# Optimization experiments

Measured on AMD Instinct MI355X. Metric: run time of the kernel, lower is better.

## Reference

```python
import jax, jax.numpy as jnp
import numpy as np

B, S, E, HID, NTR, NCAL, CW, VOCAB, POS = 4096, 201, 32, 512, 4, 8, 16, 32, 256
LN_EPS = 1e-5


def _ln(x, g, b):
    m = x.mean(-1, keepdims=True)
    v = ((x - m) ** 2).mean(-1, keepdims=True)
    return (x - m) * jax.lax.rsqrt(v + LN_EPS) * g + b


def setup_inputs() -> dict:
    key = jax.random.key(0)
    ks = jax.random.split(key, 24)
    g = lambda i, shape, s=0.1: (jax.random.normal(ks[i], shape, jnp.float32) * s)
    return dict(
        encoded_seq=jax.random.randint(ks[0], (B, S), 0, VOCAB, jnp.int32),
        experiment_id=jax.random.randint(ks[1], (B,), 0, NCAL, jnp.int32),
        tok_emb=g(2, (VOCAB, E), 1.0),
        pos_emb=g(3, (POS, E), 1.0),
        ln1_g=jnp.ones((NTR, E)), ln1_b=jnp.zeros((NTR, E)),
        wq=g(4, (NTR, E, E)), wk=g(5, (NTR, E, E)), wv=g(6, (NTR, E, E)),
        bq=g(7, (NTR, E), 0.01), bk=g(8, (NTR, E), 0.01), bv=g(9, (NTR, E), 0.01),
        wo=g(10, (NTR, E, E)), bo=g(11, (NTR, E), 0.01),
        ln2_g=jnp.ones((NTR, E)), ln2_b=jnp.zeros((NTR, E)),
        w1=g(12, (NTR, E, HID)), b1=g(13, (NTR, HID), 0.01),
        w2=g(14, (NTR, HID, E)), b2=g(15, (NTR, E), 0.01),
        lnf_g=jnp.ones((E,)), lnf_b=jnp.zeros((E,)),
        wpen=g(16, (E, 1)), bpen=g(17, (1,), 0.01),
        wfan=g(18, (1, CW)), bfan=g(19, (CW,), 0.01),
        wcal=g(20, (NCAL, CW, 1)), bcal=g(21, (NCAL, 1), 0.01),
    )


def reference(encoded_seq, experiment_id, tok_emb, pos_emb,
              ln1_g, ln1_b, wq, wk, wv, bq, bk, bv, wo, bo,
              ln2_g, ln2_b, w1, b1, w2, b2,
              lnf_g, lnf_b, wpen, bpen, wfan, bfan, wcal, bcal):
    # embedding + positional add: [B,S,E]
    x = tok_emb[encoded_seq] + pos_emb[jnp.arange(S)]
    scale = 1.0 / jnp.sqrt(jnp.float32(E))  # num_heads=1 => head_dim=E
    for i in range(NTR):
        n = _ln(x, ln1_g[i], ln1_b[i])
        q = n @ wq[i] + bq[i]
        k = n @ wk[i] + bk[i]
        v = n @ wv[i] + bv[i]
        a = jax.nn.softmax(jnp.einsum('bqe,bke->bqk', q, k) * scale, axis=-1)
        att = jnp.einsum('bqk,bke->bqe', a, v) @ wo[i] + bo[i]
        x = x + att
        h = _ln(x, ln2_g[i], ln2_b[i])
        x = x + (jax.nn.silu(h @ w1[i] + b1[i]) @ w2[i] + b2[i])
    contrib = _ln(x, lnf_g, lnf_b) @ wpen + bpen        # [B,S,1]
    underlying = contrib.sum(axis=-2)                    # [B,1]
    pre = jax.nn.elu(underlying @ wfan + bfan)           # [B,CW]
    # all calibrator heads at once: [B,NCAL]
    all_corr = jnp.einsum('bc,ncj->bn', pre, wcal) + bcal[:, 0]
    mask = jax.nn.one_hot(experiment_id, NCAL, dtype=pre.dtype)  # exactly the (exp==id) mask-sum
    corrected = (all_corr * mask).sum(-1, keepdims=True) + underlying
    return corrected.squeeze()
```

## Files before the change

### kernel.cpp

```cpp
#include <hip/hip_runtime.h>


#define SS   201
#define SP   208
#define NMT  13
#define EE   32
#define HIDN 512
#define NTRL 4
#define CWN  16
#define BB   4096
#define XST  36
#define QST  36
#define MST  72
#define VWST 228

#define X_OFF    0
#define K_OFF    14976
#define VWT_OFF  29952
#define QS_OFF   44544
#define MS_OFF   49152
#define RS_OFF   49984
#define BIAS_OFF 50816
#define SMEM_SZ  51840

#define WS_FRAG  0
#define WS_BIAS  294912
#define WS_B1    299008
#define WS_FIN   307200
#define L2E      1.4426950408889634f

typedef unsigned short u16;
typedef unsigned int   u32;
typedef short bf16x4 __attribute__((ext_vector_type(4)));
typedef short bf16x8 __attribute__((ext_vector_type(8)));
typedef float f32x4  __attribute__((ext_vector_type(4)));
typedef float f32x2  __attribute__((ext_vector_type(2)));

#define CBAR asm volatile("" ::: "memory")

__device__ __forceinline__ f32x4 MF(bf16x8 a, bf16x8 b, f32x4 c){
  return __builtin_amdgcn_mfma_f32_16x16x32_bf16(a, b, c, 0, 0, 0);
}
__device__ __forceinline__ float bf2f(u16 u){ return __uint_as_float(((u32)u)<<16); }
__device__ __forceinline__ u16 f2bf(float f){
  u32 u = __float_as_uint(f);
  u += 0x7fffu + ((u>>16)&1u);
  return (u16)(u>>16);
}
__device__ __forceinline__ u16 f2bf_fast(float f){
  return (u16)((__float_as_uint(f) + 0x8000u) >> 16);
}
__device__ __forceinline__ u32 pk2bf(f32x2 v){
#if defined(__has_builtin) && __has_builtin(__builtin_amdgcn_cvt_pk_bf16_f32)
  auto r = __builtin_amdgcn_cvt_pk_bf16_f32(v.x, v.y);
  u32 u; __builtin_memcpy(&u, &r, 4); return u;
#else
  return ((__float_as_uint(v.x)+0x8000u)>>16) | ((__float_as_uint(v.y)+0x8000u) & 0xffff0000u);
#endif
}
__device__ __forceinline__ f32x2 upk2(u32 d){
  return f32x2{ __uint_as_float(d<<16), __uint_as_float(d & 0xffff0000u) };
}
template<bool F32>
__device__ __forceinline__ float ldv(const void* p, int i){
  if (F32) return ((const float*)p)[i];
  return bf2f(((const u16*)p)[i]);
}
template<bool F32>
__device__ __forceinline__ u16 ldbf(const void* p, int i){
  if (F32) return f2bf(((const float*)p)[i]);
  return ((const u16*)p)[i];
}
__device__ __forceinline__ bf16x8 ld8(const u16* p){
  const bf16x4* q = (const bf16x4*)p;
  bf16x4 lo = q[0], hi = q[1];
  bf16x8 r = {lo[0],lo[1],lo[2],lo[3],hi[0],hi[1],hi[2],hi[3]};
  return r;
}

__device__ __forceinline__ int sniff_bf16(const void* tok_emb, int tid){
  int sane = 0;
  if (tid < 64){
    u16 wd = ((const u16*)tok_emb)[tid];
    int e = (wd >> 7) & 0xFF;
    sane = (e >= 100 && e <= 140) ? 1 : 0;
  }
  return (__syncthreads_count(sane) >= 52) ? 1 : 0;
}

template<bool F32>
__device__ __forceinline__ void frag_body(const void* wq, const void* wk,
    const void* wv, const void* wo, const void* w1, const void* w2, void* ws)
{
  int t = blockIdx.x;
  int l = t / 72, k = t % 72;
  int lane = threadIdx.x, l16 = lane & 15, quad = lane >> 4;
  bf16x8 v;
  if (k < 8){
    int mat = k >> 1, half = k & 1;
    if (mat == 2){
      int col = half*16 + l16;
      #pragma unroll
      for (int j=0;j<8;j++){
        int a = quad*8 + j;
        float acc = 0.f;
        for (int e=0;e<EE;e++)
          acc += ldv<F32>(wv, l*1024 + a*32 + e) * ldv<F32>(wo, l*1024 + e*32 + col);
        v[j] = (short)f2bf(acc);
      }
    } else {
      const void* src = (mat==0)? wq : (mat==1)? wk : wo;
      #pragma unroll
      for (int j=0;j<8;j++)
        v[j] = (short)ldbf<F32>(src, l*1024 + (quad*8+j)*32 + half*16 + l16);
    }
  } else if (k < 40){
    int nt = k - 8;
    #pragma unroll
    for (int j=0;j<8;j++)
      v[j] = (short)ldbf<F32>(w1, l*16384 + (quad*8+j)*512 + nt*16 + l16);
  } else {
    int kc = (k-40)>>1, nh = (k-40)&1;
    #pragma unroll
    for (int j=0;j<8;j++)
      v[j] = (short)ldbf<F32>(w2, l*16384 + (kc*32+quad*8+j)*32 + nh*16 + l16);
  }
  *(bf16x8*)((char*)ws + WS_FRAG + t*1024 + lane*16) = v;
}

__global__ __launch_bounds__(64) void fmt_frags(
    const void* __restrict__ tok_emb,
    const void* __restrict__ wq, const void* __restrict__ wk,
    const void* __restrict__ wv, const void* __restrict__ wo,
    const void* __restrict__ w1, const void* __restrict__ w2,
    void* __restrict__ ws)
{
  if (sniff_bf16(tok_emb, threadIdx.x)) frag_body<false>(wq,wk,wv,wo,w1,w2,ws);
  else                                  frag_body<true >(wq,wk,wv,wo,w1,w2,ws);
}

template<bool F32>
__device__ __forceinline__ void bias_body(
    const void* bq, const void* bk, const void* bv, const void* wo, const void* bo,
    const void* ln1_g, const void* ln1_b, const void* ln2_g, const void* ln2_b,
    const void* b1, const void* b2,
    const void* lnf_g, const void* lnf_b, const void* wpen, const void* bpen,
    const void* wfan, const void* bfan, const void* wcal, const void* bcal,
    void* ws)
{
  int tid = threadIdx.x, idx = tid & 31, grp = tid >> 5;
  float* BW  = (float*)((char*)ws + WS_BIAS);
  float* BW1 = (float*)((char*)ws + WS_B1);
  float* FW  = (float*)((char*)ws + WS_FIN);
  for (int l=0;l<NTRL;l++){
    float v = 0.f;
    switch(grp){
      case 0: v = ldv<F32>(bq, l*32+idx); break;
      case 1: v = ldv<F32>(bk, l*32+idx); break;
      case 2: {
        float acc = ldv<F32>(bo, l*32+idx);
        for (int e=0;e<EE;e++) acc += ldv<F32>(bv, l*32+e) * ldv<F32>(wo, l*1024 + e*32 + idx);
        v = acc; break;
      }
      case 3: v = ldv<F32>(ln1_g, l*32+idx); break;
      case 4: v = ldv<F32>(ln1_b, l*32+idx); break;
      case 5: v = ldv<F32>(ln2_g, l*32+idx); break;
      case 6: v = ldv<F32>(ln2_b, l*32+idx); break;
      case 7: v = ldv<F32>(b2,   l*32+idx); break;
    }
    BW[l*256 + tid] = v;
  }
  for (int i=tid; i<NTRL*HIDN; i+=256) BW1[i] = ldv<F32>(b1, i);
  if (tid < 32){
    FW[tid]    = ldv<F32>(lnf_g, tid);
    FW[32+tid] = ldv<F32>(lnf_b, tid);
    FW[64+tid] = ldv<F32>(wpen, tid);
  }
  if (tid == 0) FW[96] = ldv<F32>(bpen, 0);
  if (tid < 16){ FW[97+tid] = ldv<F32>(wfan, tid); FW[113+tid] = ldv<F32>(bfan, tid); }
  if (tid < 128) FW[129+tid] = ldv<F32>(wcal, tid);
  if (tid < 8)   FW[257+tid] = ldv<F32>(bcal, tid);
}

__global__ __launch_bounds__(256) void fmt_bias(
    const void* __restrict__ tok_emb,
    const void* __restrict__ bq, const void* __restrict__ bk,
    const void* __restrict__ bv, const void* __restrict__ wo, const void* __restrict__ bo,
    const void* __restrict__ ln1_g, const void* __restrict__ ln1_b,
    const void* __restrict__ ln2_g, const void* __restrict__ ln2_b,
    const void* __restrict__ b1, const void* __restrict__ b2,
    const void* __restrict__ lnf_g, const void* __restrict__ lnf_b,
    const void* __restrict__ wpen, const void* __restrict__ bpen,
    const void* __restrict__ wfan, const void* __restrict__ bfan,
    const void* __restrict__ wcal, const void* __restrict__ bcal,
    void* __restrict__ ws)
{
  if (sniff_bf16(tok_emb, threadIdx.x))
    bias_body<false>(bq,bk,bv,wo,bo,ln1_g,ln1_b,ln2_g,ln2_b,b1,b2,
                     lnf_g,lnf_b,wpen,bpen,wfan,bfan,wcal,bcal,ws);
  else
    bias_body<true >(bq,bk,bv,wo,bo,ln1_g,ln1_b,ln2_g,ln2_b,b1,b2,
                     lnf_g,lnf_b,wpen,bpen,wfan,bfan,wcal,bcal,ws);
}

__device__ __forceinline__ void ln_stats(const u16* Xb, float* MS, float* RS, int tid){
  if (tid < SP){
    const u32* row = (const u32*)(Xb + tid*XST);
    f32x2 v[16]; f32x2 s2 = {0.f,0.f};
    #pragma unroll
    for (int i=0;i<16;i++){ f32x2 p = upk2(row[i]); v[i] = p; s2 += p; }
    float m = (s2.x + s2.y) * (1.f/EE);
    f32x2 m2 = {m, m};
    f32x2 var2 = {0.f,0.f};
    #pragma unroll
    for (int i=0;i<16;i++){ f32x2 d = v[i]-m2; var2 += d*d; }
    MS[tid] = m;
    RS[tid] = rsqrtf((var2.x+var2.y)*(1.f/EE) + 1e-5f);
  }
}

__device__ __forceinline__ bf16x8 build_nfrag(const u16* Xb, const float* MS, const float* RS,
                                              int row, int quad, const f32x2* G2, const f32x2* B2){
  const u32* raw = (const u32*)(Xb + row*XST + quad*8);
  f32x2 m2 = { MS[row], MS[row] };
  f32x2 rs2 = { RS[row], RS[row] };
  u32 o[4];
  #pragma unroll
  for (int p=0;p<4;p++){
    f32x2 x = upk2(raw[p]);
    o[p] = pk2bf((x - m2) * rs2 * G2[p] + B2[p]);
  }
  bf16x8 r; __builtin_memcpy(&r, o, 16);
  return r;
}

template<bool F32>
__device__ __forceinline__ void tr_body(
    const int* seq, const int* expid,
    const void* tok_emb, const void* pos_emb,
    const void* ws, void* out, unsigned char* smem)
{
  u16*   Xb   = (u16*)(smem + X_OFF);
  u16*   Kb   = (u16*)(smem + K_OFF);
  u16*   VWTb = (u16*)(smem + VWT_OFF);
  u16*   QSb  = (u16*)(smem + QS_OFF);
  float* MS   = (float*)(smem + MS_OFF);
  float* RS   = (float*)(smem + RS_OFF);
  float* BIAS = (float*)(smem + BIAS_OFF);

  const int tid  = threadIdx.x;
  const int lane = tid & 63, w = tid >> 6;
  const int l16  = lane & 15, quad = lane >> 4;
  const int b    = blockIdx.x;
  const f32x4 Z  = {0.f,0.f,0.f,0.f};
  u16* qs = QSb + w*576;
  u16* qm = (u16*)(smem + VWT_OFF) + w*1152;

  {
    const int* srow = seq + b*SS;
    for (int i = tid; i < SP*EE; i += 256){
      int s = i >> 5, e = i & 31;
      float val = 0.f;
      if (s < SS){
        int tok = srow[s];
        val = ldv<F32>(tok_emb, tok*EE + e) + ldv<F32>(pos_emb, s*EE + e);
      }
      Xb[s*XST + e] = f2bf(val);
    }
  }
  __syncthreads();

  const float qce = 0.2550546813f;
  const f32x2 qce2 = {qce, qce};
  const f32x2 one2 = {1.f, 1.f};
  const f32x2 nl2e2 = {-L2E, -L2E};

  for (int l = 0; l < NTRL; ++l){
    const char* wsl = (const char*)ws + WS_FRAG + l*73728;
    bf16x8 bwq0 = *(const bf16x8*)(wsl + 0*1024 + lane*16);
    bf16x8 bwq1 = *(const bf16x8*)(wsl + 1*1024 + lane*16);
    bf16x8 bwk0 = *(const bf16x8*)(wsl + 2*1024 + lane*16);
    bf16x8 bwk1 = *(const bf16x8*)(wsl + 3*1024 + lane*16);
    bf16x8 bwv0 = *(const bf16x8*)(wsl + 4*1024 + lane*16);
    bf16x8 bwv1 = *(const bf16x8*)(wsl + 5*1024 + lane*16);
    {
      const float* BW = (const float*)((const char*)ws + WS_BIAS) + l*256;
      BIAS[tid] = BW[tid];
    }
    for (int i = tid; i < 32*16; i += 256)
      VWTb[(i>>4)*VWST + 208 + (i&15)] = 0;
    ln_stats(Xb, MS, RS, tid);
    __syncthreads();

    bf16x8 aq[4];
    {
      f32x2 G2[4], B2[4];
      #pragma unroll
      for (int p=0;p<4;p++){
        G2[p] = f32x2{BIAS[96+quad*8+2*p], BIAS[96+quad*8+2*p+1]};
        B2[p] = f32x2{BIAS[128+quad*8+2*p], BIAS[128+quad*8+2*p+1]};
      }
      f32x2 bqb2 = {BIAS[l16],    BIAS[16+l16]};
      f32x2 bkb2 = {BIAS[32+l16], BIAS[48+l16]};
      #pragma unroll
      for (int t=0;t<4;t++){
        int m = w + 4*t;
        if (m < NMT){
          int m16 = m*16;
          bf16x8 an = build_nfrag(Xb, MS, RS, m16+l16, quad, G2, B2);
          f32x4 ck0 = MF(an, bwk0, Z), ck1 = MF(an, bwk1, Z);
          #pragma unroll
          for (int r=0;r<4;r++){
            int row = m16 + quad*4 + r;
            u32 pk = pk2bf(f32x2{ck0[r], ck1[r]} + bkb2);
            Kb[row*XST + l16]      = (u16)pk;
            Kb[row*XST + 16 + l16] = (u16)(pk>>16);
          }
          f32x4 cw0 = MF(an, bwv0, Z), cw1 = MF(an, bwv1, Z);
          #pragma unroll
          for (int r=0;r<4;r++){
            u32 pk = pk2bf(f32x2{cw0[r], cw1[r]});
            VWTb[l16*VWST      + m16 + quad*4 + r] = (u16)pk;
            VWTb[(16+l16)*VWST + m16 + quad*4 + r] = (u16)(pk>>16);
          }
          f32x4 cq0 = MF(an, bwq0, Z), cq1 = MF(an, bwq1, Z);
          #pragma unroll
          for (int r=0;r<4;r++){
            u32 pk = pk2bf((f32x2{cq0[r], cq1[r]} + bqb2) * qce2);
            qs[(quad*4+r)*QST + l16]      = (u16)pk;
            qs[(quad*4+r)*QST + 16 + l16] = (u16)(pk>>16);
          }
          CBAR;
          aq[t] = ld8(qs + l16*QST + quad*8);
          CBAR;
        }
      }
    }
    __syncthreads();

    {
      f32x2 OB2 = {BIAS[64+l16], BIAS[80+l16]};
      #pragma unroll
      for (int t=0;t<4;t++){
        int m = w + 4*t;
        if (m < NMT){
          int m16 = m*16;
          f32x4 S[13];
          #pragma unroll
          for (int j=0;j<13;j++){
            bf16x8 kb8 = ld8(Kb + (j*16+l16)*XST + quad*8);
            S[j] = MF(aq[t], kb8, Z);
          }
          f32x2 sa = {0.f,0.f}, sb = {0.f,0.f};
          #pragma unroll
          for (int j=0;j<13;j++){
            float e0 = __builtin_amdgcn_exp2f(S[j][0]);
            float e1 = __builtin_amdgcn_exp2f(S[j][1]);
            float e2 = __builtin_amdgcn_exp2f(S[j][2]);
            float e3 = __builtin_amdgcn_exp2f(S[j][3]);
            if (j==12 && l16 >= 9){ e0=0.f; e1=0.f; e2=0.f; e3=0.f; }
            S[j] = f32x4{e0,e1,e2,e3};
            sa += f32x2{e0,e1}; sb += f32x2{e2,e3};
          }
          float sm[4] = {sa.x, sa.y, sb.x, sb.y};
          #pragma unroll
          for (int d=1; d<16; d<<=1){
            #pragma unroll
            for (int r=0;r<4;r++) sm[r] += __shfl_xor(sm[r], d);
          }
          float inv[4];
          #pragma unroll
          for (int r=0;r<4;r++) inv[r] = __builtin_amdgcn_rcpf(sm[r]);

          f32x4 o0 = Z, o1 = Z;
          #pragma unroll
          for (int c=0;c<7;c++){
            #pragma unroll
            for (int jj=0;jj<2;jj++){
              int j = 2*c + jj;
              u32 pk0 = 0, pk1 = 0;
              if (j < 13){
                pk0 = pk2bf(f32x2{S[j][0], S[j][1]});
                pk1 = pk2bf(f32x2{S[j][2], S[j][3]});
              }
              qs[(quad*4+0)*QST + jj*16 + l16] = (u16)pk0;
              qs[(quad*4+1)*QST + jj*16 + l16] = (u16)(pk0>>16);
              qs[(quad*4+2)*QST + jj*16 + l16] = (u16)pk1;
              qs[(quad*4+3)*QST + jj*16 + l16] = (u16)(pk1>>16);
            }
            CBAR;
            bf16x8 ap  = ld8(qs + l16*QST + quad*8);
            bf16x8 b0  = ld8(VWTb + l16*VWST      + c*32 + quad*8);
            bf16x8 b1f = ld8(VWTb + (16+l16)*VWST + c*32 + quad*8);
            o0 = MF(ap, b0, o0); o1 = MF(ap, b1f, o1);
            CBAR;
          }
          #pragma unroll
          for (int r=0;r<4;r++){
            int row = m16 + quad*4 + r;
            u16* x0 = Xb + row*XST + l16;
            u16* x1 = Xb + row*XST + 16 + l16;
            f32x2 xv = { bf2f(*x0), bf2f(*x1) };
            f32x2 iv = { inv[r], inv[r] };
            f32x2 ov = f32x2{o0[r], o1[r]} * iv + (xv + OB2);
            u32 pk = pk2bf(ov);
            *x0 = (u16)pk; *x1 = (u16)(pk>>16);
          }
        }
      }
    }
    __syncthreads();

    ln_stats(Xb, MS, RS, tid);
    __syncthreads();

    {
      f32x2 G2[4], B2[4];
      #pragma unroll
      for (int p=0;p<4;p++){
        G2[p] = f32x2{BIAS[160+quad*8+2*p], BIAS[160+quad*8+2*p+1]};
        B2[p] = f32x2{BIAS[192+quad*8+2*p], BIAS[192+quad*8+2*p+1]};
      }
      bf16x8 anc[4];
      #pragma unroll
      for (int t=0;t<4;t++){
        int m = w + 4*t;
        if (m < NMT) anc[t] = build_nfrag(Xb, MS, RS, m*16+l16, quad, G2, B2);
      }
      f32x4 oacc[4][2];
      #pragma unroll
      for (int t=0;t<4;t++){ oacc[t][0] = Z; oacc[t][1] = Z; }
      const char* w1f = wsl + 8*1024;
      const char* w2f = wsl + 40*1024;
      const float* BW1 = (const float*)((const char*)ws + WS_B1) + l*HIDN;

      for (int hc = 0; hc < HIDN; hc += 64){
        bf16x8 bw1[4], bw2[2][2];
        #pragma unroll
        for (int nt=0;nt<4;nt++)
          bw1[nt] = *(const bf16x8*)(w1f + (hc/16 + nt)*1024 + lane*16);
        #pragma unroll
        for (int kc=0;kc<2;kc++){
          bw2[kc][0] = *(const bf16x8*)(w2f + ((hc/32 + kc)*2    )*1024 + lane*16);
          bw2[kc][1] = *(const bf16x8*)(w2f + ((hc/32 + kc)*2 + 1)*1024 + lane*16);
        }
        f32x2 b1v2[4];
        #pragma unroll
        for (int nt=0;nt<4;nt++){
          float bb = BW1[hc + nt*16 + l16];
          b1v2[nt] = f32x2{bb, bb};
        }
        #pragma unroll
        for (int t=0;t<4;t++){
          int m = w + 4*t;
          if (m < NMT){
            #pragma unroll
            for (int nt=0;nt<4;nt++){
              f32x4 h = MF(anc[t], bw1[nt], Z);
              #pragma unroll
              for (int rp=0;rp<2;rp++){
                f32x2 z = f32x2{h[2*rp], h[2*rp+1]} + b1v2[nt];
                f32x2 a = z * nl2e2;
                f32x2 e = { __builtin_amdgcn_exp2f(a.x), __builtin_amdgcn_exp2f(a.y) };
                f32x2 d = one2 + e;
                f32x2 rc = { __builtin_amdgcn_rcpf(d.x), __builtin_amdgcn_rcpf(d.y) };
                f32x2 s = z * rc;
                u32 pk = pk2bf(s);
                qm[(quad*4+2*rp  )*MST + nt*16 + l16] = (u16)pk;
                qm[(quad*4+2*rp+1)*MST + nt*16 + l16] = (u16)(pk>>16);
              }
            }
            CBAR;
            bf16x8 ah0 = ld8(qm + l16*MST + quad*8);
            bf16x8 ah1 = ld8(qm + l16*MST + 32 + quad*8);
            oacc[t][0] = MF(ah0, bw2[0][0], oacc[t][0]);
            oacc[t][0] = MF(ah1, bw2[1][0], oacc[t][0]);
            oacc[t][1] = MF(ah0, bw2[0][1], oacc[t][1]);
            oacc[t][1] = MF(ah1, bw2[1][1], oacc[t][1]);
            CBAR;
          }
        }
      }

      f32x2 b2v2 = {BIAS[224+l16], BIAS[240+l16]};
      #pragma unroll
      for (int t=0;t<4;t++){
        int m = w + 4*t;
        if (m < NMT){
          int m16 = m*16;
          #pragma unroll
          for (int r=0;r<4;r++){
            int row = m16 + quad*4 + r;
            u16* x0 = Xb + row*XST + l16;
            u16* x1 = Xb + row*XST + 16 + l16;
            f32x2 xv = { bf2f(*x0), bf2f(*x1) };
            f32x2 ov = f32x2{oacc[t][0][r], oacc[t][1][r]} + (xv + b2v2);
            u32 pk = pk2bf(ov);
            *x0 = (u16)pk; *x1 = (u16)(pk>>16);
          }
        }
      }
    }
    __syncthreads();
  }

  const float* FW = (const float*)((const char*)ws + WS_FIN);
  if (tid < 32){
    BIAS[tid]    = FW[tid];
    BIAS[32+tid] = FW[32+tid];
    BIAS[64+tid] = FW[64+tid];
  }
  __syncthreads();
  float part = 0.f;
  if (tid < SS){
    const u32* row = (const u32*)(Xb + tid*XST);
    f32x2 v[16]; f32x2 s2 = {0.f,0.f};
    #pragma unroll
    for (int i=0;i<16;i++){ f32x2 p = upk2(row[i]); v[i] = p; s2 += p; }
    float m = (s2.x+s2.y) * (1.f/EE);
    f32x2 m2 = {m,m};
    f32x2 var2 = {0.f,0.f};
    #pragma unroll
    for (int i=0;i<16;i++){ f32x2 d = v[i]-m2; var2 += d*d; }
    float rs = rsqrtf((var2.x+var2.y)*(1.f/EE) + 1e-5f);
    f32x2 rs2 = {rs, rs};
    f32x2 dot2 = {0.f,0.f};
    #pragma unroll
    for (int i=0;i<16;i++){
      f32x2 g  = {BIAS[2*i], BIAS[2*i+1]};
      f32x2 bb = {BIAS[32+2*i], BIAS[33+2*i]};
      f32x2 wp = {BIAS[64+2*i], BIAS[65+2*i]};
      dot2 += ((v[i]-m2)*rs2*g + bb) * wp;
    }
    part = dot2.x + dot2.y + FW[96];
  }
  #pragma unroll
  for (int off=32; off; off>>=1) part += __shfl_xor(part, off);
  float* REDF = (float*)(smem + QS_OFF);
  __syncthreads();
  if (lane == 0) REDF[w] = part;
  __syncthreads();
  if (tid == 0){
    float u = REDF[0] + REDF[1] + REDF[2] + REDF[3];
    int ex = expid[b];
    float corr = FW[257+ex];
    #pragma unroll
    for (int c = 0; c < CWN; ++c){
      float pre = u * FW[97+c] + FW[113+c];
      pre = pre > 0.f ? pre : (__expf(pre) - 1.f);
      corr += pre * FW[129 + ex*CWN + c];
    }
    float res = corr + u;
    if (F32) ((float*)out)[b] = res;
    else     ((u16*)out)[b]  = f2bf(res);
  }
}

__global__ __launch_bounds__(256, 3) void tr_kernel(
    const int* __restrict__ seq, const int* __restrict__ expid,
    const void* __restrict__ tok_emb, const void* __restrict__ pos_emb,
    const void* __restrict__ ws, void* __restrict__ out)
{
  __shared__ __align__(16) unsigned char smem[SMEM_SZ];
  if (sniff_bf16(tok_emb, threadIdx.x))
    tr_body<false>(seq, expid, tok_emb, pos_emb, ws, out, smem);
  else
    tr_body<true >(seq, expid, tok_emb, pos_emb, ws, out, smem);
}

extern "C" void kernel_launch(void* const* d_in, const int* in_sizes, int n_in,
                              void* d_out, int out_size, void* d_ws, size_t ws_size,
                              hipStream_t stream)
{
  (void)in_sizes; (void)n_in; (void)ws_size; (void)out_size;
  const void* tok_emb = d_in[2];
  fmt_frags<<<dim3(288), dim3(64), 0, stream>>>(
      tok_emb, d_in[6], d_in[7], d_in[8], d_in[12], d_in[16], d_in[18], d_ws);
  fmt_bias<<<dim3(1), dim3(256), 0, stream>>>(
      tok_emb, d_in[9], d_in[10], d_in[11], d_in[12], d_in[13],
      d_in[4], d_in[5], d_in[14], d_in[15], d_in[17], d_in[19],
      d_in[20], d_in[21], d_in[22], d_in[23],
      d_in[24], d_in[25], d_in[26], d_in[27], d_ws);
  tr_kernel<<<dim3(BB), dim3(256), 0, stream>>>(
      (const int*)d_in[0], (const int*)d_in[1], tok_emb, d_in[3], d_ws, d_out);
}
```

Measured before the change: 996.2 us.

## Keep attention probabilities in registers via transposed MFMA, drop LDS round-trip

Computes the score tile transposed (K as A operand) so each lane's exponentiated probabilities already sit in the B-operand layout for the P·V MFMA. They are packed to bf16 in registers, removing the per-chunk LDS staging of P and its two barriers per chunk. The row-sum reduction shrinks to two cross-quad shuffles, and the residual update uses packed 32-bit accesses. The LDS reads of V are split into two 4-element halves to match the new operand order, which may add LDS instructions or bank conflicts.

```diff
diff --git a/kernel.cpp b/kernel.cpp
--- a/kernel.cpp
+++ b/kernel.cpp
@@ -76,6 +76,14 @@
   bf16x4 lo = q[0], hi = q[1];
   bf16x8 r = {lo[0],lo[1],lo[2],lo[3],hi[0],hi[1],hi[2],hi[3]};
   return r;
+}
+__device__ __forceinline__ bf16x8 cat44(bf16x4 lo, bf16x4 hi){
+  bf16x8 r = {lo[0],lo[1],lo[2],lo[3],hi[0],hi[1],hi[2],hi[3]};
+  return r;
+}
+__device__ __forceinline__ bf16x8 mk8(u32 a0, u32 a1, u32 a2, u32 a3){
+  u32 t[4] = {a0,a1,a2,a3};
+  bf16x8 r; __builtin_memcpy(&r, t, 16); return r;
 }
 
 __device__ __forceinline__ int sniff_bf16(const void* tok_emb, int tid){
@@ -339,72 +347,73 @@
     __syncthreads();
 
     {
-      f32x2 OB2 = {BIAS[64+l16], BIAS[80+l16]};
+      const u16* vbase0 = VWTb + l16*VWST;
+      const u16* vbase1 = VWTb + (16+l16)*VWST;
+      f32x4 ob0 = *(const f32x4*)(BIAS + 64 + quad*4);
+      f32x4 ob1 = *(const f32x4*)(BIAS + 80 + quad*4);
       #pragma unroll
       for (int t=0;t<4;t++){
         int m = w + 4*t;
         if (m < NMT){
           int m16 = m*16;
-          f32x4 S[13];
+          u32 pbw[13][2];
+          float part = 0.f;
           #pragma unroll
-          for (int j=0;j<13;j++){
-            bf16x8 kb8 = ld8(Kb + (j*16+l16)*XST + quad*8);
-            S[j] = MF(aq[t], kb8, Z);
-          }
-          f32x2 sa = {0.f,0.f}, sb = {0.f,0.f};
-          #pragma unroll
-          for (int j=0;j<13;j++){
-            float e0 = __builtin_amdgcn_exp2f(S[j][0]);
-            float e1 = __builtin_amdgcn_exp2f(S[j][1]);
-            float e2 = __builtin_amdgcn_exp2f(S[j][2]);
-            float e3 = __builtin_amdgcn_exp2f(S[j][3]);
-            if (j==12 && l16 >= 9){ e0=0.f; e1=0.f; e2=0.f; e3=0.f; }
-            S[j] = f32x4{e0,e1,e2,e3};
-            sa += f32x2{e0,e1}; sb += f32x2{e2,e3};
-          }
-          float sm[4] = {sa.x, sa.y, sb.x, sb.y};
-          #pragma unroll
-          for (int d=1; d<16; d<<=1){
-            #pragma unroll
-            for (int r=0;r<4;r++) sm[r] += __shfl_xor(sm[r], d);
-          }
-          float inv[4];
-          #pragma unroll
-          for (int r=0;r<4;r++) inv[r] = __builtin_amdgcn_rcpf(sm[r]);
+          for (int kt=0; kt<13; kt++){
+            bf16x8 kb8 = ld8(Kb + (kt*16+l16)*XST + quad*8);
+            f32x4 St = MF(kb8, aq[t], Z);
+            float e0 = __builtin_amdgcn_exp2f(St[0]);
+            float e1 = __builtin_amdgcn_exp2f(St[1]);
+            float e2 = __builtin_amdgcn_exp2f(St[2]);
+            float e3 = __builtin_amdgcn_exp2f(St[3]);
+            if (kt == 12){
+              int kb = quad*4;
+              if (kb+0 >= 9) e0 = 0.f;
+              if (kb+1 >= 9) e1 = 0.f;
+              if (kb+2 >= 9) e2 = 0.f;
+              if (kb+3 >= 9) e3 = 0.f;
+            }
+            part += (e0+e1)+(e2+e3);
+            pbw[kt][0] = pk2bf(f32x2{e0,e1});
+            pbw[kt][1] = pk2bf(f32x2{e2,e3});
+          }
+          part += __shfl_xor(part, 16);
+          part += __shfl_xor(part, 32);
+          float inv = __builtin_amdgcn_rcpf(part);
 
           f32x4 o0 = Z, o1 = Z;
           #pragma unroll
-          for (int c=0;c<7;c++){
-            #pragma unroll
-            for (int jj=0;jj<2;jj++){
-              int j = 2*c + jj;
-              u32 pk0 = 0, pk1 = 0;
-              if (j < 13){
-                pk0 = pk2bf(f32x2{S[j][0], S[j][1]});
-                pk1 = pk2bf(f32x2{S[j][2], S[j][3]});
-              }
-              qs[(quad*4+0)*QST + jj*16 + l16] = (u16)pk0;
-              qs[(quad*4+1)*QST + jj*16 + l16] = (u16)(pk0>>16);
-              qs[(quad*4+2)*QST + jj*16 + l16] = (u16)pk1;
-              qs[(quad*4+3)*QST + jj*16 + l16] = (u16)(pk1>>16);
-            }
-            CBAR;
-            bf16x8 ap  = ld8(qs + l16*QST + quad*8);
-            bf16x8 b0  = ld8(VWTb + l16*VWST      + c*32 + quad*8);
-            bf16x8 b1f = ld8(VWTb + (16+l16)*VWST + c*32 + quad*8);
-            o0 = MF(ap, b0, o0); o1 = MF(ap, b1f, o1);
-            CBAR;
-          }
-          #pragma unroll
-          for (int r=0;r<4;r++){
-            int row = m16 + quad*4 + r;
-            u16* x0 = Xb + row*XST + l16;
-            u16* x1 = Xb + row*XST + 16 + l16;
-            f32x2 xv = { bf2f(*x0), bf2f(*x1) };
-            f32x2 iv = { inv[r], inv[r] };
-            f32x2 ov = f32x2{o0[r], o1[r]} * iv + (xv + OB2);
-            u32 pk = pk2bf(ov);
-            *x0 = (u16)pk; *x1 = (u16)(pk>>16);
+          for (int c=0;c<6;c++){
+            bf16x4 a0l = *(const bf16x4*)(vbase0 + c*32 + quad*4);
+            bf16x4 a0h = *(const bf16x4*)(vbase0 + c*32 + 16 + quad*4);
+            bf16x4 a1l = *(const bf16x4*)(vbase1 + c*32 + quad*4);
+            bf16x4 a1h = *(const bf16x4*)(vbase1 + c*32 + 16 + quad*4);
+            bf16x8 B8 = mk8(pbw[2*c][0], pbw[2*c][1], pbw[2*c+1][0], pbw[2*c+1][1]);
+            o0 = MF(cat44(a0l, a0h), B8, o0);
+            o1 = MF(cat44(a1l, a1h), B8, o1);
+          }
+          {
+            bf16x4 a0l = *(const bf16x4*)(vbase0 + 192 + quad*4);
+            bf16x4 a0h = *(const bf16x4*)(vbase0 + 208 + quad*4);
+            bf16x4 a1l = *(const bf16x4*)(vbase1 + 192 + quad*4);
+            bf16x4 a1h = *(const bf16x4*)(vbase1 + 208 + quad*4);
+            bf16x8 B8 = mk8(pbw[12][0], pbw[12][1], 0u, 0u);
+            o0 = MF(cat44(a0l, a0h), B8, o0);
+            o1 = MF(cat44(a1l, a1h), B8, o1);
+          }
+
+          u32* xr = (u32*)(Xb + (m16+l16)*XST);
+          {
+            u32 d0 = xr[quad*2], d1 = xr[quad*2+1];
+            f32x2 r01 = f32x2{o0[0],o0[1]} * inv + (upk2(d0) + f32x2{ob0[0],ob0[1]});
+            f32x2 r23 = f32x2{o0[2],o0[3]} * inv + (upk2(d1) + f32x2{ob0[2],ob0[3]});
+            xr[quad*2]   = pk2bf(r01);
+            xr[quad*2+1] = pk2bf(r23);
+            u32 d2 = xr[8+quad*2], d3 = xr[8+quad*2+1];
+            f32x2 s01 = f32x2{o1[0],o1[1]} * inv + (upk2(d2) + f32x2{ob1[0],ob1[1]});
+            f32x2 s23 = f32x2{o1[2],o1[3]} * inv + (upk2(d3) + f32x2{ob1[2],ob1[3]});
+            xr[8+quad*2]   = pk2bf(s01);
+            xr[8+quad*2+1] = pk2bf(s23);
           }
         }
       }
```

Result: faster. 923.4 us (-7.3%).
